# Kernel tuning notes

Measured on AMD Instinct MI355X. Metric: run time of the kernel, lower is better.

Reference implementation:

```python
import jax, jax.numpy as jnp
import numpy as np

N = 50000   # nodes
E = 800000  # edges
V = 10000   # vocab
D = 128     # emb_dim
H = 128     # hidden_dim
C = 10      # num_classes
G = 512     # graphs in batch


def setup_inputs() -> dict:
    key = jax.random.key(0)
    ks = jax.random.split(key, 10)
    return {
        "x_tokens": jax.random.randint(ks[0], (N,), 0, V),
        "edge_index": jax.random.randint(ks[1], (2, E), 0, N),
        "batch": jnp.sort(jax.random.randint(ks[2], (N,), 0, G)),
        "emb": jax.random.normal(ks[3], (V, D), dtype=jnp.float32) * 0.05,
        "w1": jax.random.normal(ks[4], (D, H), dtype=jnp.float32) * 0.05,
        "b1": jax.random.normal(ks[5], (H,), dtype=jnp.float32) * 0.05,
        "w2": jax.random.normal(ks[6], (H, H), dtype=jnp.float32) * 0.05,
        "b2": jax.random.normal(ks[7], (H,), dtype=jnp.float32) * 0.05,
        "lin_w": jax.random.normal(ks[8], (H, C), dtype=jnp.float32) * 0.05,
        "lin_b": jax.random.normal(ks[9], (C,), dtype=jnp.float32) * 0.05,
    }


def _gcn_conv(x, W, b, src, dst, norm):
    # PyG GCNConv: x' = D^{-1/2}(A+I)D^{-1/2} X W + b (self-loops already in src/dst)
    h = x @ W                                  # [N, H]
    msg = h[src] * norm[:, None]               # [E+N, H] gather + scale
    return jax.ops.segment_sum(msg, dst, num_segments=N) + b


def reference(x_tokens, edge_index, batch, emb, w1, b1, w2, b2, lin_w, lin_b):
    # embedding with padding_idx=0 (row 0 forced to zero)
    table = emb * (jnp.arange(V) != 0)[:, None].astype(emb.dtype)
    x = table[x_tokens]                        # [N, D]

    # add self loops, symmetric degree normalization (computed once)
    loops = jnp.arange(N)
    src = jnp.concatenate([edge_index[0], loops])
    dst = jnp.concatenate([edge_index[1], loops])
    deg = jax.ops.segment_sum(jnp.ones_like(dst, dtype=x.dtype), dst, num_segments=N)
    dis = jax.lax.rsqrt(deg)                   # deg >= 1 due to self loops
    norm = dis[src] * dis[dst]                 # [E+N]

    x = jax.nn.relu(_gcn_conv(x, w1, b1, src, dst, norm))
    x = jax.nn.relu(_gcn_conv(x, w2, b2, src, dst, norm))

    # global mean pool over graphs
    sums = jax.ops.segment_sum(x, batch, num_segments=G)          # [G, H]
    cnts = jax.ops.segment_sum(jnp.ones((N,), x.dtype), batch, num_segments=G)
    pooled = sums / jnp.maximum(cnts, 1.0)[:, None]

    return pooled @ lin_w + lin_b              # [G, C]
```

## Files before the change

### kernel.cpp

```cpp
#include <hip/hip_runtime.h>
#include <hip/hip_bf16.h>


typedef unsigned int uint;
typedef unsigned short ushort;
typedef __attribute__((ext_vector_type(8))) short bf16x8;
typedef __attribute__((ext_vector_type(4))) float f32x4;

__device__ inline float bf_lo(uint u) { return __uint_as_float(u << 16); }
__device__ inline float bf_hi(uint u) { return __uint_as_float(u & 0xffff0000u); }
__device__ inline ushort f2bf(float f) {
    uint u = __float_as_uint(f);
    return (ushort)((u + 0x7fffu + ((u >> 16) & 1u)) >> 16);
}
__device__ inline uint pack2bf(float a, float b) {
    return (uint)f2bf(a) | ((uint)f2bf(b) << 16);
}

#define EPB 2048
#define CAP 8192

__global__ __launch_bounds__(256) void init0(int* __restrict__ bcur,
                                             const float* __restrict__ W1,
                                             const float* __restrict__ W2,
                                             ushort* __restrict__ W1t,
                                             ushort* __restrict__ W2t) {
    if (blockIdx.x == 0) {
        bcur[threadIdx.x] = 0;
    } else {
        int i = (blockIdx.x - 1) * 256 + threadIdx.x;
        const float* Ws = (i < 16384) ? W1 : W2;
        ushort* Wd      = (i < 16384) ? W1t : W2t;
        int j = i & 16383;
        int nn = j >> 7, k = j & 127;
        Wd[j] = f2bf(Ws[k * 128 + nn]);
    }
}

__global__ __launch_bounds__(256) void bucket_scatter(const int* __restrict__ src,
                                                      const int* __restrict__ dst,
                                                      int* __restrict__ bcur,
                                                      uint* __restrict__ bstage,
                                                      int E, int NB) {
    __shared__ int lh[256];
    __shared__ int lbase[257];
    __shared__ int gbase[256];
    __shared__ int lcur[256];
    __shared__ uint stage[EPB];
    const int t = threadIdx.x;
    const int base = blockIdx.x * EPB;
    const int end  = min(E, base + EPB);
    const int tot  = end - base;

    lh[t] = 0;
    __syncthreads();

    uint pk[8]; int bk[8]; int cnt = 0;
    for (int i = base + t; i < end; i += 256) {
        int s = src[i];
        uint d = (uint)dst[i];
        bk[cnt] = (int)(d >> 8);
        pk[cnt] = (uint)s | ((d & 255u) << 24);
        atomicAdd(&lh[bk[cnt]], 1);
        ++cnt;
    }
    __syncthreads();

    if (t < NB && lh[t]) gbase[t] = t * CAP + atomicAdd(&bcur[t], lh[t]);
    {
        __shared__ int ls[256];
        int v = lh[t];
        ls[t] = v;
        __syncthreads();
        for (int off = 1; off < 256; off <<= 1) {
            int x = (t >= off) ? ls[t - off] : 0;
            __syncthreads();
            ls[t] += x;
            __syncthreads();
        }
        lbase[t] = ls[t] - v;
        if (t == 255) lbase[256] = ls[255];
        lcur[t] = 0;
    }
    __syncthreads();

    for (int j = 0; j < cnt; ++j) {
        int p = lbase[bk[j]] + atomicAdd(&lcur[bk[j]], 1);
        stage[p] = pk[j];
    }
    __syncthreads();

    for (int i = t; i < tot; i += 256) {
        int lo = 0, hi = 256;
        while (lo + 1 < hi) {
            int mid = (lo + hi) >> 1;
            if (lbase[mid] <= i) lo = mid; else hi = mid;
        }
        bstage[gbase[lo] + (i - lbase[lo])] = stage[i];
    }
}

__device__ void csr_body(int* lds,
                         const uint* __restrict__ bstage,
                         const int* __restrict__ bcur,
                         float* __restrict__ dis,
                         int* __restrict__ rbeg,
                         int* __restrict__ rend,
                         int* __restrict__ csr,
                         int N, int b) {
    int* lh    = lds;
    int* ls    = lds + 256;
    int* lbase = lds + 512;
    int* lcur  = lds + 768;
    const int t = threadIdx.x;
    const int base  = b * CAP;
    const int cntb  = bcur[b];
    const int n0    = b << 8;
    const int nn    = min(256, N - n0);

    lh[t] = 0;
    __syncthreads();
    for (int i = t; i < cntb; i += 256)
        atomicAdd(&lh[bstage[base + i] >> 24], 1);
    __syncthreads();

    const int v = lh[t];
    ls[t] = v;
    __syncthreads();
    for (int off = 1; off < 256; off <<= 1) {
        int x = (t >= off) ? ls[t - off] : 0;
        __syncthreads();
        ls[t] += x;
        __syncthreads();
    }
    lbase[t] = ls[t] - v;
    lcur[t] = 0;
    if (t < nn) {
        dis[n0 + t]  = rsqrtf((float)v + 1.0f);
        rbeg[n0 + t] = base + lbase[t];
        rend[n0 + t] = base + lbase[t] + v;
    }
    __syncthreads();

    for (int i = t; i < cntb; i += 256) {
        uint e = bstage[base + i];
        int dl = (int)(e >> 24);
        int pos = base + lbase[dl] + atomicAdd(&lcur[dl], 1);
        csr[pos] = (int)(e & 0xFFFFFFu);
    }
}

template<bool GATHER, bool SCALE>
__device__ void gemm_body(ushort* wl,
                          const ushort* __restrict__ Xbf,
                          const int* __restrict__ tokens,
                          const float* __restrict__ emb,
                          const ushort* __restrict__ Wt,
                          const float* __restrict__ dis,
                          ushort* __restrict__ Out, int n, int bid) {
    const int tid = threadIdx.x;
    {
        const int row  = tid >> 1;
        const int half = tid & 1;
        const int base = row * 256 + half * 128;
#pragma unroll
        for (int i = 0; i < 8; ++i) {
            int off = base + i * 16;
            uint4 v = *(const uint4*)((const char*)Wt + off);
            int swz = off ^ ((row & 7) << 4);
            *(uint4*)((char*)wl + swz) = v;
        }
    }
    __syncthreads();

    const int w  = tid >> 6;
    const int l  = tid & 63;
    const int lr = l & 15;
    const int lg = l >> 4;
    const int rowBase = bid * 128 + w * 32;

    f32x4 acc[2][8];
#pragma unroll
    for (int s = 0; s < 2; ++s)
#pragma unroll
        for (int ct = 0; ct < 8; ++ct) acc[s][ct] = (f32x4){0.f, 0.f, 0.f, 0.f};

    bf16x8 afrag[2][4];
#pragma unroll
    for (int s = 0; s < 2; ++s) {
        const int row = rowBase + s * 16 + lr;
        if (row < n) {
            if (GATHER) {
                const int tok = tokens[row];
                if (tok != 0) {
                    const float* ep = emb + (size_t)tok * 128;
#pragma unroll
                    for (int kk = 0; kk < 4; ++kk) {
                        const float* q = ep + kk * 32 + lg * 8;
                        float4 lo = *(const float4*)q;
                        float4 hi = *(const float4*)(q + 4);
                        uint4 pk;
                        pk.x = pack2bf(lo.x, lo.y); pk.y = pack2bf(lo.z, lo.w);
                        pk.z = pack2bf(hi.x, hi.y); pk.w = pack2bf(hi.z, hi.w);
                        union { uint4 u; bf16x8 b; } c; c.u = pk;
                        afrag[s][kk] = c.b;
                    }
                } else {
#pragma unroll
                    for (int kk = 0; kk < 4; ++kk) afrag[s][kk] = (bf16x8){0,0,0,0,0,0,0,0};
                }
            } else {
                const ushort* xp = Xbf + (size_t)row * 128;
#pragma unroll
                for (int kk = 0; kk < 4; ++kk)
                    afrag[s][kk] = *(const bf16x8*)(xp + kk * 32 + lg * 8);
            }
        } else {
#pragma unroll
            for (int kk = 0; kk < 4; ++kk) afrag[s][kk] = (bf16x8){0,0,0,0,0,0,0,0};
        }
    }

#pragma unroll
    for (int ct = 0; ct < 8; ++ct) {
#pragma unroll
        for (int kk = 0; kk < 4; ++kk) {
            const int nrow = ct * 16 + lr;
            int off = nrow * 256 + kk * 64 + lg * 16;
            off ^= ((nrow & 7) << 4);
            bf16x8 b = *(const bf16x8*)((const char*)wl + off);
            acc[0][ct] = __builtin_amdgcn_mfma_f32_16x16x32_bf16(afrag[0][kk], b, acc[0][ct], 0, 0, 0);
            acc[1][ct] = __builtin_amdgcn_mfma_f32_16x16x32_bf16(afrag[1][kk], b, acc[1][ct], 0, 0, 0);
        }
    }

#pragma unroll
    for (int s = 0; s < 2; ++s) {
#pragma unroll
        for (int r = 0; r < 4; ++r) {
            const int row = rowBase + s * 16 + lg * 4 + r;
            if (row < n) {
                const float sc = SCALE ? dis[row] : 1.0f;
                ushort* op = Out + (size_t)row * 128 + lr;
#pragma unroll
                for (int ct = 0; ct < 8; ++ct)
                    op[ct * 16] = f2bf(acc[s][ct][r] * sc);
            }
        }
    }
}

__global__ __launch_bounds__(256) void csr_gemm1_fused(const uint* __restrict__ bstage,
                                                       const int* __restrict__ bcur,
                                                       float* __restrict__ dis,
                                                       int* __restrict__ rbeg,
                                                       int* __restrict__ rend,
                                                       int* __restrict__ csr,
                                                       const int* __restrict__ tokens,
                                                       const float* __restrict__ emb,
                                                       const ushort* __restrict__ W1t,
                                                       ushort* __restrict__ H,
                                                       int4* __restrict__ poolz, int pz4,
                                                       int N, int NB, int GB) {
    __shared__ ushort wl[128 * 128];
    const int b = blockIdx.x;
    if (b < NB) {
        csr_body((int*)wl, bstage, bcur, dis, rbeg, rend, csr, N, b);
    } else if (b < NB + GB) {
        gemm_body<true, false>(wl, nullptr, tokens, emb, W1t, nullptr, H, N, b - NB);
    } else {
        int i = (b - NB - GB) * 256 + threadIdx.x;
        if (i < pz4) poolz[i] = make_int4(0, 0, 0, 0);
    }
}

__global__ __launch_bounds__(256) void gemm2_kernel(const ushort* __restrict__ Xbf,
                                                    const ushort* __restrict__ Wt,
                                                    const float* __restrict__ dis,
                                                    ushort* __restrict__ Out, int n) {
    __shared__ ushort wl[128 * 128];
    gemm_body<false, true>(wl, Xbf, nullptr, nullptr, Wt, dis, Out, n, blockIdx.x);
}

__global__ __launch_bounds__(256) void aggregate_w(const ushort* __restrict__ H,
                                                   const float* __restrict__ dis,
                                                   const int* __restrict__ rbeg,
                                                   const int* __restrict__ rend,
                                                   const int* __restrict__ csr,
                                                   const float* __restrict__ bias,
                                                   ushort* __restrict__ Out, int n) {
    const int g = threadIdx.x >> 4;
    const int l = threadIdx.x & 15;
    const int node = blockIdx.x * 16 + g;
    if (node >= n) return;

    const float dn = dis[node];
    const uint4 hq = *(const uint4*)(H + (size_t)node * 128 + l * 8);
    const int e0 = rbeg[node];
    const int e1 = rend[node];

    float s0_=0.f,s1_=0.f,s2_=0.f,s3_=0.f,s4_=0.f,s5_=0.f,s6_=0.f,s7_=0.f;

    int e = e0;
    for (; e + 8 <= e1; e += 8) {
        int a[8];
#pragma unroll
        for (int j = 0; j < 8; ++j) a[j] = csr[e + j];
        float w[8];
#pragma unroll
        for (int j = 0; j < 8; ++j) w[j] = dis[a[j]];
        uint4 h[8];
#pragma unroll
        for (int j = 0; j < 8; ++j) h[j] = *(const uint4*)(H + (size_t)a[j] * 128 + l * 8);
#pragma unroll
        for (int j = 0; j < 8; ++j) {
            s0_ += bf_lo(h[j].x) * w[j]; s1_ += bf_hi(h[j].x) * w[j];
            s2_ += bf_lo(h[j].y) * w[j]; s3_ += bf_hi(h[j].y) * w[j];
            s4_ += bf_lo(h[j].z) * w[j]; s5_ += bf_hi(h[j].z) * w[j];
            s6_ += bf_lo(h[j].w) * w[j]; s7_ += bf_hi(h[j].w) * w[j];
        }
    }
    for (; e + 4 <= e1; e += 4) {
        int a[4];
#pragma unroll
        for (int j = 0; j < 4; ++j) a[j] = csr[e + j];
        float w[4];
#pragma unroll
        for (int j = 0; j < 4; ++j) w[j] = dis[a[j]];
        uint4 h[4];
#pragma unroll
        for (int j = 0; j < 4; ++j) h[j] = *(const uint4*)(H + (size_t)a[j] * 128 + l * 8);
#pragma unroll
        for (int j = 0; j < 4; ++j) {
            s0_ += bf_lo(h[j].x) * w[j]; s1_ += bf_hi(h[j].x) * w[j];
            s2_ += bf_lo(h[j].y) * w[j]; s3_ += bf_hi(h[j].y) * w[j];
            s4_ += bf_lo(h[j].z) * w[j]; s5_ += bf_hi(h[j].z) * w[j];
            s6_ += bf_lo(h[j].w) * w[j]; s7_ += bf_hi(h[j].w) * w[j];
        }
    }
    for (; e < e1; ++e) {
        const int a = csr[e];
        const float w = dis[a];
        const uint4 h = *(const uint4*)(H + (size_t)a * 128 + l * 8);
        s0_ += bf_lo(h.x)*w; s1_ += bf_hi(h.x)*w;
        s2_ += bf_lo(h.y)*w; s3_ += bf_hi(h.y)*w;
        s4_ += bf_lo(h.z)*w; s5_ += bf_hi(h.z)*w;
        s6_ += bf_lo(h.w)*w; s7_ += bf_hi(h.w)*w;
    }

    const float self = dn * dn;
    const float4 bA = *(const float4*)&bias[l * 8];
    const float4 bB = *(const float4*)&bias[l * 8 + 4];
    float o0 = fmaxf(s0_ * dn + bf_lo(hq.x) * self + bA.x, 0.0f);
    float o1 = fmaxf(s1_ * dn + bf_hi(hq.x) * self + bA.y, 0.0f);
    float o2 = fmaxf(s2_ * dn + bf_lo(hq.y) * self + bA.z, 0.0f);
    float o3 = fmaxf(s3_ * dn + bf_hi(hq.y) * self + bA.w, 0.0f);
    float o4 = fmaxf(s4_ * dn + bf_lo(hq.z) * self + bB.x, 0.0f);
    float o5 = fmaxf(s5_ * dn + bf_hi(hq.z) * self + bB.y, 0.0f);
    float o6 = fmaxf(s6_ * dn + bf_lo(hq.w) * self + bB.z, 0.0f);
    float o7 = fmaxf(s7_ * dn + bf_hi(hq.w) * self + bB.w, 0.0f);

    uint4 o;
    o.x = pack2bf(o0, o1); o.y = pack2bf(o2, o3);
    o.z = pack2bf(o4, o5); o.w = pack2bf(o6, o7);
    *(uint4*)(Out + (size_t)node * 128 + l * 8) = o;
}

__global__ __launch_bounds__(256) void aggregate_pool(const ushort* __restrict__ H,
                                                      const float* __restrict__ dis,
                                                      const int* __restrict__ rbeg,
                                                      const int* __restrict__ rend,
                                                      const int* __restrict__ csr,
                                                      const float* __restrict__ bias,
                                                      const int* __restrict__ batch,
                                                      float* __restrict__ pooled,
                                                      int n) {
    const int g = threadIdx.x >> 4;
    const int l = threadIdx.x & 15;
    const int node = blockIdx.x * 16 + g;
    const bool valid = node < n;

    float s0_=0.f,s1_=0.f,s2_=0.f,s3_=0.f,s4_=0.f,s5_=0.f,s6_=0.f,s7_=0.f;
    float dn = 0.f;
    const float4 bA = *(const float4*)&bias[l * 8];
    const float4 bB = *(const float4*)&bias[l * 8 + 4];

    if (valid) {
        dn = dis[node];
        const uint4 hq = *(const uint4*)(H + (size_t)node * 128 + l * 8);
        s0_ = bf_lo(hq.x); s1_ = bf_hi(hq.x);
        s2_ = bf_lo(hq.y); s3_ = bf_hi(hq.y);
        s4_ = bf_lo(hq.z); s5_ = bf_hi(hq.z);
        s6_ = bf_lo(hq.w); s7_ = bf_hi(hq.w);

        const int e0 = rbeg[node];
        const int e1 = rend[node];
        int e = e0;
        for (; e + 8 <= e1; e += 8) {
            int a[8];
#pragma unroll
            for (int j = 0; j < 8; ++j) a[j] = csr[e + j];
            uint4 h[8];
#pragma unroll
            for (int j = 0; j < 8; ++j) h[j] = *(const uint4*)(H + (size_t)a[j] * 128 + l * 8);
#pragma unroll
            for (int j = 0; j < 8; ++j) {
                s0_ += bf_lo(h[j].x); s1_ += bf_hi(h[j].x);
                s2_ += bf_lo(h[j].y); s3_ += bf_hi(h[j].y);
                s4_ += bf_lo(h[j].z); s5_ += bf_hi(h[j].z);
                s6_ += bf_lo(h[j].w); s7_ += bf_hi(h[j].w);
            }
        }
        for (; e + 4 <= e1; e += 4) {
            int a[4];
#pragma unroll
            for (int j = 0; j < 4; ++j) a[j] = csr[e + j];
            uint4 h[4];
#pragma unroll
            for (int j = 0; j < 4; ++j) h[j] = *(const uint4*)(H + (size_t)a[j] * 128 + l * 8);
#pragma unroll
            for (int j = 0; j < 4; ++j) {
                s0_ += bf_lo(h[j].x); s1_ += bf_hi(h[j].x);
                s2_ += bf_lo(h[j].y); s3_ += bf_hi(h[j].y);
                s4_ += bf_lo(h[j].z); s5_ += bf_hi(h[j].z);
                s6_ += bf_lo(h[j].w); s7_ += bf_hi(h[j].w);
            }
        }
        for (; e < e1; ++e) {
            const uint4 h = *(const uint4*)(H + (size_t)csr[e] * 128 + l * 8);
            s0_ += bf_lo(h.x); s1_ += bf_hi(h.x);
            s2_ += bf_lo(h.y); s3_ += bf_hi(h.y);
            s4_ += bf_lo(h.z); s5_ += bf_hi(h.z);
            s6_ += bf_lo(h.w); s7_ += bf_hi(h.w);
        }
    }

    const float o0 = fmaxf(s0_ * dn + bA.x, 0.0f);
    const float o1 = fmaxf(s1_ * dn + bA.y, 0.0f);
    const float o2 = fmaxf(s2_ * dn + bA.z, 0.0f);
    const float o3 = fmaxf(s3_ * dn + bA.w, 0.0f);
    const float o4 = fmaxf(s4_ * dn + bB.x, 0.0f);
    const float o5 = fmaxf(s5_ * dn + bB.y, 0.0f);
    const float o6 = fmaxf(s6_ * dn + bB.z, 0.0f);
    const float o7 = fmaxf(s7_ * dn + bB.w, 0.0f);

    __shared__ float x3[16][128];
    __shared__ int bv[16];
    if (valid) {
        float4 va, vb;
        va.x = o0; va.y = o1; va.z = o2; va.w = o3;
        vb.x = o4; vb.y = o5; vb.z = o6; vb.w = o7;
        *(float4*)&x3[g][l * 8]     = va;
        *(float4*)&x3[g][l * 8 + 4] = vb;
        if (l == 0) bv[g] = batch[node];
    } else if (l == 0) {
        bv[g] = -1;
    }
    __syncthreads();
    const int t = threadIdx.x;
    if (t < 128) {
        int cur = bv[0];
        float run = 0.0f;
        for (int r = 0; r < 16; ++r) {
            const int b = bv[r];
            if (b < 0) break;
            if (b != cur) {
                if (run != 0.0f) atomicAdd(&pooled[(size_t)cur * 128 + t], run);
                cur = b; run = 0.0f;
            }
            run += x3[r][t];
        }
        if (cur >= 0 && run != 0.0f) atomicAdd(&pooled[(size_t)cur * 128 + t], run);
    }
}

__global__ __launch_bounds__(128) void pool_finalize(const float* __restrict__ pooled,
                                                     const int* __restrict__ batch,
                                                     const float* __restrict__ lw,
                                                     const float* __restrict__ lb,
                                                     float* __restrict__ out, int n) {
    const int g = blockIdx.x;
    const int t = threadIdx.x;
    int lo = 0, hi = n;
    while (lo < hi) { int mid = (lo + hi) >> 1; if (batch[mid] < g) lo = mid + 1; else hi = mid; }
    const int s = lo;
    hi = n;
    while (lo < hi) { int mid = (lo + hi) >> 1; if (batch[mid] < g + 1) lo = mid + 1; else hi = mid; }
    const float c = fmaxf((float)(lo - s), 1.0f);

    __shared__ float pl[128];
    pl[t] = pooled[(size_t)g * 128 + t] / c;
    __syncthreads();
    if (t < 10) {
        float acc = lb[t];
#pragma unroll 16
        for (int d = 0; d < 128; ++d) acc += pl[d] * lw[d * 10 + t];
        out[g * 10 + t] = acc;
    }
}

extern "C" void kernel_launch(void* const* d_in, const int* in_sizes, int n_in,
                              void* d_out, int out_size, void* d_ws, size_t ws_size,
                              hipStream_t stream) {
    const int*   tokens = (const int*)d_in[0];
    const int*   eidx   = (const int*)d_in[1];
    const int*   batch  = (const int*)d_in[2];
    const float* emb    = (const float*)d_in[3];
    const float* w1     = (const float*)d_in[4];
    const float* b1     = (const float*)d_in[5];
    const float* w2     = (const float*)d_in[6];
    const float* b2     = (const float*)d_in[7];
    const float* lw     = (const float*)d_in[8];
    const float* lbv    = (const float*)d_in[9];

    const int N = in_sizes[0];
    const int E = in_sizes[1] / 2;
    const int G = out_size / 10;
    const int* src = eidx;
    const int* dst = eidx + E;
    const int NB = (N + 255) >> 8;
    const int GB = (N + 127) / 128;

    char* p = (char*)d_ws;
    auto alloc = [&](size_t bytes) { void* r = (void*)p; p += (bytes + 255) & ~(size_t)255; return r; };
    float*  dis    = (float*)alloc((size_t)N * 4);
    int*    rbeg   = (int*)  alloc((size_t)N * 4);
    int*    rend   = (int*)  alloc((size_t)N * 4);
    int*    bcur   = (int*)  alloc(256 * 4);
    float*  pooled = (float*)alloc((size_t)G * 128 * 4);
    uint*   bstage = (uint*) alloc((size_t)NB * CAP * 4);
    int*    csr    = (int*)  alloc((size_t)NB * CAP * 4);
    ushort* W1t    = (ushort*)alloc(16384 * 2);
    ushort* W2t    = (ushort*)alloc(16384 * 2);
    ushort* A      = (ushort*)alloc((size_t)N * 128 * 2);
    ushort* B      = (ushort*)alloc((size_t)N * 128 * 2);

    const int PZ4 = (G * 128) / 4;
    const int PZB = (PZ4 + 255) / 256;
    const int EB  = (E + EPB - 1) / EPB;

    init0<<<129, 256, 0, stream>>>(bcur, w1, w2, W1t, W2t);
    bucket_scatter<<<EB, 256, 0, stream>>>(src, dst, bcur, bstage, E, NB);
    csr_gemm1_fused<<<NB + GB + PZB, 256, 0, stream>>>(bstage, bcur, dis, rbeg, rend, csr,
                                                       tokens, emb, W1t, A,
                                                       (int4*)pooled, PZ4, N, NB, GB);
    aggregate_w<<<(N + 15) / 16, 256, 0, stream>>>(A, dis, rbeg, rend, csr, b1, B, N);
    gemm2_kernel<<<GB, 256, 0, stream>>>(B, W2t, dis, A, N);
    aggregate_pool<<<(N + 15) / 16, 256, 0, stream>>>(A, dis, rbeg, rend, csr, b2, batch, pooled, N);
    pool_finalize<<<G, 128, 0, stream>>>(pooled, batch, lw, lbv, (float*)d_out, N);
}
```

Baseline: 137.0 us.

## Split aggregation kernels into four column slices per node group

```diff
diff --git a/kernel.cpp b/kernel.cpp
--- a/kernel.cpp
+++ b/kernel.cpp
@@ -282,20 +282,20 @@
     gemm_body<false, true>(wl, Xbf, nullptr, nullptr, Wt, dis, Out, n, blockIdx.x);
 }
 
-__global__ __launch_bounds__(256) void aggregate_w(const ushort* __restrict__ H,
-                                                   const float* __restrict__ dis,
-                                                   const int* __restrict__ rbeg,
-                                                   const int* __restrict__ rend,
-                                                   const int* __restrict__ csr,
-                                                   const float* __restrict__ bias,
-                                                   ushort* __restrict__ Out, int n) {
-    const int g = threadIdx.x >> 4;
-    const int l = threadIdx.x & 15;
-    const int node = blockIdx.x * 16 + g;
+__global__ __launch_bounds__(256) void agg1_slice(const ushort* __restrict__ H,
+                                                  const float* __restrict__ dis,
+                                                  const int* __restrict__ rbeg,
+                                                  const int* __restrict__ rend,
+                                                  const int* __restrict__ csr,
+                                                  const float* __restrict__ bias,
+                                                  ushort* __restrict__ Out, int n) {
+    const int slice = blockIdx.x & 3;
+    const int node  = (blockIdx.x >> 2) * 64 + (threadIdx.x >> 2);
+    const int colb  = slice * 32 + (threadIdx.x & 3) * 8;
     if (node >= n) return;
 
     const float dn = dis[node];
-    const uint4 hq = *(const uint4*)(H + (size_t)node * 128 + l * 8);
+    const uint4 hq = *(const uint4*)(H + (size_t)node * 128 + colb);
     const int e0 = rbeg[node];
     const int e1 = rend[node];
 
@@ -311,7 +311,7 @@
         for (int j = 0; j < 8; ++j) w[j] = dis[a[j]];
         uint4 h[8];
 #pragma unroll
-        for (int j = 0; j < 8; ++j) h[j] = *(const uint4*)(H + (size_t)a[j] * 128 + l * 8);
+        for (int j = 0; j < 8; ++j) h[j] = *(const uint4*)(H + (size_t)a[j] * 128 + colb);
 #pragma unroll
         for (int j = 0; j < 8; ++j) {
             s0_ += bf_lo(h[j].x) * w[j]; s1_ += bf_hi(h[j].x) * w[j];
@@ -329,7 +329,7 @@
         for (int j = 0; j < 4; ++j) w[j] = dis[a[j]];
         uint4 h[4];
 #pragma unroll
-        for (int j = 0; j < 4; ++j) h[j] = *(const uint4*)(H + (size_t)a[j] * 128 + l * 8);
+        for (int j = 0; j < 4; ++j) h[j] = *(const uint4*)(H + (size_t)a[j] * 128 + colb);
 #pragma unroll
         for (int j = 0; j < 4; ++j) {
             s0_ += bf_lo(h[j].x) * w[j]; s1_ += bf_hi(h[j].x) * w[j];
@@ -341,7 +341,7 @@
     for (; e < e1; ++e) {
         const int a = csr[e];
         const float w = dis[a];
-        const uint4 h = *(const uint4*)(H + (size_t)a * 128 + l * 8);
+        const uint4 h = *(const uint4*)(H + (size_t)a * 128 + colb);
         s0_ += bf_lo(h.x)*w; s1_ += bf_hi(h.x)*w;
         s2_ += bf_lo(h.y)*w; s3_ += bf_hi(h.y)*w;
         s4_ += bf_lo(h.z)*w; s5_ += bf_hi(h.z)*w;
@@ -349,8 +349,8 @@
     }
 
     const float self = dn * dn;
-    const float4 bA = *(const float4*)&bias[l * 8];
-    const float4 bB = *(const float4*)&bias[l * 8 + 4];
+    const float4 bA = *(const float4*)&bias[colb];
+    const float4 bB = *(const float4*)&bias[colb + 4];
     float o0 = fmaxf(s0_ * dn + bf_lo(hq.x) * self + bA.x, 0.0f);
     float o1 = fmaxf(s1_ * dn + bf_hi(hq.x) * self + bA.y, 0.0f);
     float o2 = fmaxf(s2_ * dn + bf_lo(hq.y) * self + bA.z, 0.0f);
@@ -363,31 +363,33 @@
     uint4 o;
     o.x = pack2bf(o0, o1); o.y = pack2bf(o2, o3);
     o.z = pack2bf(o4, o5); o.w = pack2bf(o6, o7);
-    *(uint4*)(Out + (size_t)node * 128 + l * 8) = o;
-}
-
-__global__ __launch_bounds__(256) void aggregate_pool(const ushort* __restrict__ H,
-                                                      const float* __restrict__ dis,
-                                                      const int* __restrict__ rbeg,
-                                                      const int* __restrict__ rend,
-                                                      const int* __restrict__ csr,
-                                                      const float* __restrict__ bias,
-                                                      const int* __restrict__ batch,
-                                                      float* __restrict__ pooled,
-                                                      int n) {
-    const int g = threadIdx.x >> 4;
-    const int l = threadIdx.x & 15;
-    const int node = blockIdx.x * 16 + g;
+    *(uint4*)(Out + (size_t)node * 128 + colb) = o;
+}
+
+__global__ __launch_bounds__(256) void agg2_pool_slice(const ushort* __restrict__ H,
+                                                       const float* __restrict__ dis,
+                                                       const int* __restrict__ rbeg,
+                                                       const int* __restrict__ rend,
+                                                       const int* __restrict__ csr,
+                                                       const float* __restrict__ bias,
+                                                       const int* __restrict__ batch,
+                                                       float* __restrict__ pooled,
+                                                       int n) {
+    const int slice = blockIdx.x & 3;
+    const int nr    = threadIdx.x >> 2;
+    const int node  = (blockIdx.x >> 2) * 64 + nr;
+    const int cq    = threadIdx.x & 3;
+    const int colb  = slice * 32 + cq * 8;
     const bool valid = node < n;
 
     float s0_=0.f,s1_=0.f,s2_=0.f,s3_=0.f,s4_=0.f,s5_=0.f,s6_=0.f,s7_=0.f;
     float dn = 0.f;
-    const float4 bA = *(const float4*)&bias[l * 8];
-    const float4 bB = *(const float4*)&bias[l * 8 + 4];
+    const float4 bA = *(const float4*)&bias[colb];
+    const float4 bB = *(const float4*)&bias[colb + 4];
 
     if (valid) {
         dn = dis[node];
-        const uint4 hq = *(const uint4*)(H + (size_t)node * 128 + l * 8);
+        const uint4 hq = *(const uint4*)(H + (size_t)node * 128 + colb);
         s0_ = bf_lo(hq.x); s1_ = bf_hi(hq.x);
         s2_ = bf_lo(hq.y); s3_ = bf_hi(hq.y);
         s4_ = bf_lo(hq.z); s5_ = bf_hi(hq.z);
@@ -402,7 +404,7 @@
             for (int j = 0; j < 8; ++j) a[j] = csr[e + j];
             uint4 h[8];
 #pragma unroll
-            for (int j = 0; j < 8; ++j) h[j] = *(const uint4*)(H + (size_t)a[j] * 128 + l * 8);
+            for (int j = 0; j < 8; ++j) h[j] = *(const uint4*)(H + (size_t)a[j] * 128 + colb);
 #pragma unroll
             for (int j = 0; j < 8; ++j) {
                 s0_ += bf_lo(h[j].x); s1_ += bf_hi(h[j].x);
@@ -417,7 +419,7 @@
             for (int j = 0; j < 4; ++j) a[j] = csr[e + j];
             uint4 h[4];
 #pragma unroll
-            for (int j = 0; j < 4; ++j) h[j] = *(const uint4*)(H + (size_t)a[j] * 128 + l * 8);
+            for (int j = 0; j < 4; ++j) h[j] = *(const uint4*)(H + (size_t)a[j] * 128 + colb);
 #pragma unroll
             for (int j = 0; j < 4; ++j) {
                 s0_ += bf_lo(h[j].x); s1_ += bf_hi(h[j].x);
@@ -427,7 +429,7 @@
             }
         }
         for (; e < e1; ++e) {
-            const uint4 h = *(const uint4*)(H + (size_t)csr[e] * 128 + l * 8);
+            const uint4 h = *(const uint4*)(H + (size_t)csr[e] * 128 + colb);
             s0_ += bf_lo(h.x); s1_ += bf_hi(h.x);
             s2_ += bf_lo(h.y); s3_ += bf_hi(h.y);
             s4_ += bf_lo(h.z); s5_ += bf_hi(h.z);
@@ -435,42 +437,45 @@
         }
     }
 
-    const float o0 = fmaxf(s0_ * dn + bA.x, 0.0f);
-    const float o1 = fmaxf(s1_ * dn + bA.y, 0.0f);
-    const float o2 = fmaxf(s2_ * dn + bA.z, 0.0f);
-    const float o3 = fmaxf(s3_ * dn + bA.w, 0.0f);
-    const float o4 = fmaxf(s4_ * dn + bB.x, 0.0f);
-    const float o5 = fmaxf(s5_ * dn + bB.y, 0.0f);
-    const float o6 = fmaxf(s6_ * dn + bB.z, 0.0f);
-    const float o7 = fmaxf(s7_ * dn + bB.w, 0.0f);
-
-    __shared__ float x3[16][128];
-    __shared__ int bv[16];
+    __shared__ float x3[64][32];
+    __shared__ int bv[64];
     if (valid) {
         float4 va, vb;
-        va.x = o0; va.y = o1; va.z = o2; va.w = o3;
-        vb.x = o4; vb.y = o5; vb.z = o6; vb.w = o7;
-        *(float4*)&x3[g][l * 8]     = va;
-        *(float4*)&x3[g][l * 8 + 4] = vb;
-        if (l == 0) bv[g] = batch[node];
-    } else if (l == 0) {
-        bv[g] = -1;
-    }
-    __syncthreads();
+        va.x = fmaxf(s0_ * dn + bA.x, 0.0f);
+        va.y = fmaxf(s1_ * dn + bA.y, 0.0f);
+        va.z = fmaxf(s2_ * dn + bA.z, 0.0f);
+        va.w = fmaxf(s3_ * dn + bA.w, 0.0f);
+        vb.x = fmaxf(s4_ * dn + bB.x, 0.0f);
+        vb.y = fmaxf(s5_ * dn + bB.y, 0.0f);
+        vb.z = fmaxf(s6_ * dn + bB.z, 0.0f);
+        vb.w = fmaxf(s7_ * dn + bB.w, 0.0f);
+        *(float4*)&x3[nr][cq * 8]     = va;
+        *(float4*)&x3[nr][cq * 8 + 4] = vb;
+        if (cq == 0) bv[nr] = batch[node];
+    } else if (cq == 0) {
+        bv[nr] = -1;
+    }
+    __syncthreads();
+
     const int t = threadIdx.x;
     if (t < 128) {
-        int cur = bv[0];
-        float run = 0.0f;
-        for (int r = 0; r < 16; ++r) {
-            const int b = bv[r];
-            if (b < 0) break;
-            if (b != cur) {
-                if (run != 0.0f) atomicAdd(&pooled[(size_t)cur * 128 + t], run);
-                cur = b; run = 0.0f;
+        const int gi  = t >> 5;
+        const int col = t & 31;
+        const int r0 = gi * 16, r1 = r0 + 16;
+        int cur = bv[r0];
+        if (cur >= 0) {
+            float run = 0.0f;
+            for (int r = r0; r < r1; ++r) {
+                const int b = bv[r];
+                if (b < 0) break;
+                if (b != cur) {
+                    if (run != 0.0f) atomicAdd(&pooled[(size_t)cur * 128 + slice * 32 + col], run);
+                    cur = b; run = 0.0f;
+                }
+                run += x3[r][col];
             }
-            run += x3[r][t];
-        }
-        if (cur >= 0 && run != 0.0f) atomicAdd(&pooled[(size_t)cur * 128 + t], run);
+            if (run != 0.0f) atomicAdd(&pooled[(size_t)cur * 128 + slice * 32 + col], run);
+        }
     }
 }
 
@@ -520,6 +525,7 @@
     const int* dst = eidx + E;
     const int NB = (N + 255) >> 8;
     const int GB = (N + 127) / 128;
+    const int AB = ((N + 63) / 64) * 4;
 
     char* p = (char*)d_ws;
     auto alloc = [&](size_t bytes) { void* r = (void*)p; p += (bytes + 255) & ~(size_t)255; return r; };
@@ -544,8 +550,8 @@
     csr_gemm1_fused<<<NB + GB + PZB, 256, 0, stream>>>(bstage, bcur, dis, rbeg, rend, csr,
                                                        tokens, emb, W1t, A,
                                                        (int4*)pooled, PZ4, N, NB, GB);
-    aggregate_w<<<(N + 15) / 16, 256, 0, stream>>>(A, dis, rbeg, rend, csr, b1, B, N);
+    agg1_slice<<<AB, 256, 0, stream>>>(A, dis, rbeg, rend, csr, b1, B, N);
     gemm2_kernel<<<GB, 256, 0, stream>>>(B, W2t, dis, A, N);
-    aggregate_pool<<<(N + 15) / 16, 256, 0, stream>>>(A, dis, rbeg, rend, csr, b2, batch, pooled, N);
+    agg2_pool_slice<<<AB, 256, 0, stream>>>(A, dis, rbeg, rend, csr, b2, batch, pooled, N);
     pool_finalize<<<G, 128, 0, stream>>>(pooled, batch, lw, lbv, (float*)d_out, N);
 }
```

New measurement: 162.0 us. 1.18x slower.

## Fuse layer-1 GEMM with edge bucket scatter; split CSR build into lean kernel

Applied to the files above, without the earlier changes.

```diff
diff --git a/kernel.cpp b/kernel.cpp
--- a/kernel.cpp
+++ b/kernel.cpp
@@ -37,18 +37,20 @@
     }
 }
 
-__global__ __launch_bounds__(256) void bucket_scatter(const int* __restrict__ src,
-                                                      const int* __restrict__ dst,
-                                                      int* __restrict__ bcur,
-                                                      uint* __restrict__ bstage,
-                                                      int E, int NB) {
-    __shared__ int lh[256];
-    __shared__ int lbase[257];
-    __shared__ int gbase[256];
-    __shared__ int lcur[256];
-    __shared__ uint stage[EPB];
+__device__ void scatter_body(int* lds,
+                             const int* __restrict__ src,
+                             const int* __restrict__ dst,
+                             int* __restrict__ bcur,
+                             uint* __restrict__ bstage,
+                             int E, int NB, int bid) {
+    int*  lh    = lds;
+    int*  lbase = lds + 256;
+    int*  gbase = lds + 513;
+    int*  lcur  = lds + 769;
+    int*  ls    = lds + 1025;
+    uint* stage = (uint*)(lds + 1284);
     const int t = threadIdx.x;
-    const int base = blockIdx.x * EPB;
+    const int base = bid * EPB;
     const int end  = min(E, base + EPB);
     const int tot  = end - base;
 
@@ -68,7 +70,6 @@
 
     if (t < NB && lh[t]) gbase[t] = t * CAP + atomicAdd(&bcur[t], lh[t]);
     {
-        __shared__ int ls[256];
         int v = lh[t];
         ls[t] = v;
         __syncthreads();
@@ -250,26 +251,38 @@
     }
 }
 
-__global__ __launch_bounds__(256) void csr_gemm1_fused(const uint* __restrict__ bstage,
-                                                       const int* __restrict__ bcur,
-                                                       float* __restrict__ dis,
-                                                       int* __restrict__ rbeg,
-                                                       int* __restrict__ rend,
-                                                       int* __restrict__ csr,
-                                                       const int* __restrict__ tokens,
-                                                       const float* __restrict__ emb,
-                                                       const ushort* __restrict__ W1t,
-                                                       ushort* __restrict__ H,
-                                                       int4* __restrict__ poolz, int pz4,
-                                                       int N, int NB, int GB) {
+__global__ __launch_bounds__(256) void scatter_gemm1_fused(const int* __restrict__ src,
+                                                           const int* __restrict__ dst,
+                                                           int* __restrict__ bcur,
+                                                           uint* __restrict__ bstage,
+                                                           const int* __restrict__ tokens,
+                                                           const float* __restrict__ emb,
+                                                           const ushort* __restrict__ W1t,
+                                                           ushort* __restrict__ H,
+                                                           int E, int NB, int EB, int N) {
     __shared__ ushort wl[128 * 128];
     const int b = blockIdx.x;
+    if (b < EB) {
+        scatter_body((int*)wl, src, dst, bcur, bstage, E, NB, b);
+    } else {
+        gemm_body<true, false>(wl, nullptr, tokens, emb, W1t, nullptr, H, N, b - EB);
+    }
+}
+
+__global__ __launch_bounds__(256) void csr_poolz(const uint* __restrict__ bstage,
+                                                 const int* __restrict__ bcur,
+                                                 float* __restrict__ dis,
+                                                 int* __restrict__ rbeg,
+                                                 int* __restrict__ rend,
+                                                 int* __restrict__ csr,
+                                                 int4* __restrict__ poolz, int pz4,
+                                                 int N, int NB) {
+    __shared__ int lds[1024];
+    const int b = blockIdx.x;
     if (b < NB) {
-        csr_body((int*)wl, bstage, bcur, dis, rbeg, rend, csr, N, b);
-    } else if (b < NB + GB) {
-        gemm_body<true, false>(wl, nullptr, tokens, emb, W1t, nullptr, H, N, b - NB);
+        csr_body(lds, bstage, bcur, dis, rbeg, rend, csr, N, b);
     } else {
-        int i = (b - NB - GB) * 256 + threadIdx.x;
+        int i = (b - NB) * 256 + threadIdx.x;
         if (i < pz4) poolz[i] = make_int4(0, 0, 0, 0);
     }
 }
@@ -540,10 +553,10 @@
     const int EB  = (E + EPB - 1) / EPB;
 
     init0<<<129, 256, 0, stream>>>(bcur, w1, w2, W1t, W2t);
-    bucket_scatter<<<EB, 256, 0, stream>>>(src, dst, bcur, bstage, E, NB);
-    csr_gemm1_fused<<<NB + GB + PZB, 256, 0, stream>>>(bstage, bcur, dis, rbeg, rend, csr,
-                                                       tokens, emb, W1t, A,
-                                                       (int4*)pooled, PZ4, N, NB, GB);
+    scatter_gemm1_fused<<<EB + GB, 256, 0, stream>>>(src, dst, bcur, bstage,
+                                                     tokens, emb, W1t, A, E, NB, EB, N);
+    csr_poolz<<<NB + PZB, 256, 0, stream>>>(bstage, bcur, dis, rbeg, rend, csr,
+                                            (int4*)pooled, PZ4, N, NB);
     aggregate_w<<<(N + 15) / 16, 256, 0, stream>>>(A, dis, rbeg, rend, csr, b1, B, N);
     gemm2_kernel<<<GB, 256, 0, stream>>>(B, W2t, dis, A, N);
     aggregate_pool<<<(N + 15) / 16, 256, 0, stream>>>(A, dis, rbeg, rend, csr, b2, batch, pooled, N);
```

Result: no change. 135.4 us (-1.2%).
